# Kernel optimization log

Hardware: AMD Instinct MI355X
Metric: run time of the kernel (lower is better)

The kernel has to match this reference:

```python
import jax, jax.numpy as jnp
import numpy as np

N = 50000          # nodes
E = 800000         # edges (avg degree 16)
IN, HID, OUT = 128, 32, 64
H1, H2, H3 = 4, 4, 6
NEG_SLOPE = 0.2


def setup_inputs() -> dict:
    key = jax.random.key(0)
    ks = jax.random.split(key, 18)

    def p(k, shape, fan_in):
        return (jax.random.normal(k, shape, jnp.float32) / np.sqrt(fan_in)).astype(jnp.float32)

    return {
        "x": jax.random.normal(ks[0], (N, IN), jnp.float32),
        "src": jax.random.randint(ks[1], (E,), 0, N, jnp.int32),
        "dst": jax.random.randint(ks[2], (E,), 0, N, jnp.int32),
        # layer 1: IN -> (H1, HID)
        "W1": p(ks[3], (IN, H1 * HID), IN),
        "al1": p(ks[4], (H1, HID), HID),
        "ar1": p(ks[5], (H1, HID), HID),
        "b1": jnp.zeros((H1 * HID,), jnp.float32),
        # layer 2: H1*HID -> (H2, HID), residual (identity since H1*HID == H2*HID... == in)
        "W2": p(ks[6], (H1 * HID, H2 * HID), H1 * HID),
        "al2": p(ks[7], (H2, HID), HID),
        "ar2": p(ks[8], (H2, HID), HID),
        "b2": jnp.zeros((H2 * HID,), jnp.float32),
        # layer 3: H2*HID -> (H3, OUT), residual via linear projection
        "W3": p(ks[9], (H2 * HID, H3 * OUT), H2 * HID),
        "al3": p(ks[10], (H3, OUT), OUT),
        "ar3": p(ks[11], (H3, OUT), OUT),
        "b3": jnp.zeros((H3 * OUT,), jnp.float32),
        "Wres3": p(ks[12], (H2 * HID, H3 * OUT), H2 * HID),
    }


def _gat_layer(h, W, al, ar, b, src, dst, H, D, resval=None):
    # DGL GATConv: proj, per-edge attention logits, leaky-relu, edge softmax
    # over destination neighborhoods, weighted gather-scatter aggregation.
    feat = (h @ W).reshape(N, H, D)                     # [N,H,D]
    el = jnp.sum(feat * al, axis=-1)                    # [N,H]
    er = jnp.sum(feat * ar, axis=-1)                    # [N,H]
    e = jax.nn.leaky_relu(el[src] + er[dst], NEG_SLOPE) # [E,H]
    # numerically-stable segment softmax over dst
    m = jax.ops.segment_max(e, dst, num_segments=N)     # [N,H]
    ex = jnp.exp(e - m[dst])
    s = jax.ops.segment_sum(ex, dst, num_segments=N)    # [N,H]
    a = ex / s[dst]                                     # [E,H]
    msg = feat[src] * a[..., None]                      # [E,H,D]
    rst = jax.ops.segment_sum(msg, dst, num_segments=N) # [N,H,D]
    if resval is not None:
        rst = rst + resval
    return rst + b.reshape(1, H, D)


def reference(x, src, dst, W1, al1, ar1, b1, W2, al2, ar2, b2,
              W3, al3, ar3, b3, Wres3):
    h = jax.nn.elu(_gat_layer(x, W1, al1, ar1, b1, src, dst, H1, HID))
    h = h.reshape(N, H1 * HID)
    h2 = jax.nn.elu(_gat_layer(h, W2, al2, ar2, b2, src, dst, H2, HID,
                               resval=h.reshape(N, H2, HID)))
    h2 = h2.reshape(N, H2 * HID)
    h3 = _gat_layer(h2, W3, al3, ar3, b3, src, dst, H3, OUT,
                    resval=(h2 @ Wres3).reshape(N, H3, OUT))
    return h3.mean(axis=1)                              # [N,OUT]
```

## Files before the change

kernel.cpp:

```cpp
#include <hip/hip_runtime.h>
#include <hip/hip_bf16.h>


#define NODES 50000
#define EDGES 800000
#define NEG 0.2f

typedef __attribute__((ext_vector_type(8))) short bh8;
typedef __attribute__((ext_vector_type(4))) float f4;

__device__ __forceinline__ float leaky(float e) { return e > 0.f ? e : NEG * e; }
__device__ __forceinline__ float blo(unsigned u) { return __uint_as_float(u << 16); }
__device__ __forceinline__ float bhi(unsigned u) { return __uint_as_float(u & 0xffff0000u); }
__device__ __forceinline__ float bf2f(unsigned short u) {
    return __uint_as_float(((unsigned)u) << 16);
}
__device__ __forceinline__ unsigned f2bf(float f) {
    unsigned u = __float_as_uint(f);
    return (u + 0x7fffu + ((u >> 16) & 1u)) >> 16;
}
__device__ __forceinline__ float sel4(float4 v, int h) {
    float a = (h & 1) ? v.y : v.x;
    float b = (h & 1) ? v.w : v.z;
    return (h & 2) ? b : a;
}

#define SW(row, bc) (((row) << 8) + ((bc) ^ (((row) & 7) << 4)))

__global__ void k_cast(const float* __restrict__ in, unsigned short* __restrict__ outb, int n4) {
    int gid = blockIdx.x * blockDim.x + threadIdx.x;
    if (gid >= n4) return;
    float4 v = *reinterpret_cast<const float4*>(in + (size_t)gid * 4);
    unsigned u0 = f2bf(v.x) | (f2bf(v.y) << 16);
    unsigned u1 = f2bf(v.z) | (f2bf(v.w) << 16);
    *reinterpret_cast<uint2*>(outb + (size_t)gid * 4) = make_uint2(u0, u1);
}

__global__ void k_prepw(const float* __restrict__ W, unsigned short* __restrict__ WT, int F) {
    int gid = blockIdx.x * blockDim.x + threadIdx.x;
    if (gid >= 128 * F) return;
    int k = gid / F, f = gid - k * F;
    WT[(size_t)f * 128 + k] = (unsigned short)f2bf(W[gid]);
}

__global__ void k_hist(const int* __restrict__ dst, int* __restrict__ cnt, int e) {
    int gid = blockIdx.x * blockDim.x + threadIdx.x;
    if (gid < e) atomicAdd(&cnt[dst[gid]], 1);
}

__global__ __launch_bounds__(1024) void k_scan(const int* __restrict__ deg,
                                               int* __restrict__ offs, int n) {
    const int CH = (n + 1023) / 1024;
    int t = threadIdx.x;
    int base = t * CH;
    int s = 0;
    for (int j = 0; j < CH; ++j) {
        int i = base + j;
        if (i < n) s += deg[i];
    }
    __shared__ int sm[1024];
    sm[t] = s;
    __syncthreads();
    for (int off = 1; off < 1024; off <<= 1) {
        int v = (t >= off) ? sm[t - off] : 0;
        __syncthreads();
        sm[t] += v;
        __syncthreads();
    }
    int run = sm[t] - s;
    for (int j = 0; j < CH; ++j) {
        int i = base + j;
        if (i < n) { offs[i] = run; run += deg[i]; }
    }
    if (t == 1023) offs[n] = sm[1023];
}

__global__ void k_fill(const int* __restrict__ src, const int* __restrict__ dst,
                       const int* __restrict__ offs, int* __restrict__ cur,
                       int* __restrict__ csr, int e) {
    int gid = blockIdx.x * blockDim.x + threadIdx.x;
    if (gid < e) {
        int d = dst[gid];
        int pos = offs[d] + atomicAdd(&cur[d], 1);
        csr[pos] = src[gid];
    }
}

template <int F>
__global__ __launch_bounds__(256) void k_mgemm(const unsigned short* __restrict__ A,
                                               const unsigned short* __restrict__ BT,
                                               unsigned short* __restrict__ C0,
                                               unsigned short* __restrict__ C1,
                                               int nrows) {
    __shared__ char Alds[64 * 256];
    __shared__ char Blds[64 * 256];
    const int t  = threadIdx.x;
    const int n0 = blockIdx.x * 64;
    const int w  = t >> 6;
    const int l  = t & 63;
    const int lr = l & 15;
    const int lk = l >> 4;

    {
        int col8 = (t & 15) * 8;
        int bc   = col8 * 2;
#pragma unroll
        for (int p = 0; p < 4; ++p) {
            int row = p * 16 + (t >> 4);
            int gr  = n0 + row;
            uint4 v = make_uint4(0, 0, 0, 0);
            if (gr < nrows) v = *reinterpret_cast<const uint4*>(A + (size_t)gr * 128 + col8);
            *reinterpret_cast<uint4*>(Alds + SW(row, bc)) = v;
        }
    }

    const int rbase = (w & 1) * 32;
    const int cbase = (w >> 1) * 32;

    for (int ct = 0; ct < F / 64; ++ct) {
        __syncthreads();
        {
            int col8 = (t & 15) * 8;
            int bc   = col8 * 2;
#pragma unroll
            for (int p = 0; p < 4; ++p) {
                int row = p * 16 + (t >> 4);
                uint4 v = *reinterpret_cast<const uint4*>(BT + (size_t)(ct * 64 + row) * 128 + col8);
                *reinterpret_cast<uint4*>(Blds + SW(row, bc)) = v;
            }
        }
        __syncthreads();

        f4 acc00 = {0.f, 0.f, 0.f, 0.f}, acc01 = {0.f, 0.f, 0.f, 0.f};
        f4 acc10 = {0.f, 0.f, 0.f, 0.f}, acc11 = {0.f, 0.f, 0.f, 0.f};
#pragma unroll
        for (int kk = 0; kk < 4; ++kk) {
            int bck = kk * 64 + lk * 16;
            bh8 a0 = *reinterpret_cast<const bh8*>(Alds + SW(rbase + lr, bck));
            bh8 a1 = *reinterpret_cast<const bh8*>(Alds + SW(rbase + 16 + lr, bck));
            bh8 b0 = *reinterpret_cast<const bh8*>(Blds + SW(cbase + lr, bck));
            bh8 b1 = *reinterpret_cast<const bh8*>(Blds + SW(cbase + 16 + lr, bck));
            acc00 = __builtin_amdgcn_mfma_f32_16x16x32_bf16(a0, b0, acc00, 0, 0, 0);
            acc01 = __builtin_amdgcn_mfma_f32_16x16x32_bf16(a0, b1, acc01, 0, 0, 0);
            acc10 = __builtin_amdgcn_mfma_f32_16x16x32_bf16(a1, b0, acc10, 0, 0, 0);
            acc11 = __builtin_amdgcn_mfma_f32_16x16x32_bf16(a1, b1, acc11, 0, 0, 0);
        }

        unsigned short* dst = (F == 128) ? C0 : (ct < 6 ? C0 : C1);
        const int width  = (F == 128) ? 128 : 384;
        const int cb     = (F == 128) ? ct * 64 : (ct < 6 ? ct * 64 : ct * 64 - 384);
        const f4* accs[4] = {&acc00, &acc01, &acc10, &acc11};
#pragma unroll
        for (int m = 0; m < 2; ++m) {
#pragma unroll
            for (int j = 0; j < 4; ++j) {
                int gr = n0 + rbase + m * 16 + lk * 4 + j;
                if (gr >= nrows) continue;
#pragma unroll
                for (int n = 0; n < 2; ++n) {
                    float v = (*accs[m * 2 + n])[j];
                    dst[(size_t)gr * width + cb + cbase + n * 16 + lr] = (unsigned short)f2bf(v);
                }
            }
        }
    }
}

template <int H, int D>
__global__ void k_elr_bf(const unsigned short* __restrict__ feat,
                         const float* __restrict__ al, const float* __restrict__ ar,
                         float* __restrict__ el, float* __restrict__ er, int total) {
    int gid = blockIdx.x * blockDim.x + threadIdx.x;
    if (gid >= total) return;
    int n = gid / H, h = gid - n * H;
    const uint4* f = reinterpret_cast<const uint4*>(feat + (size_t)n * (H * D) + h * D);
    const float4* a = reinterpret_cast<const float4*>(al + h * D);
    const float4* r = reinterpret_cast<const float4*>(ar + h * D);
    float sl = 0.f, sr = 0.f;
#pragma unroll
    for (int j = 0; j < D / 8; ++j) {
        uint4 v = f[j];
        float4 a0 = a[2 * j], a1 = a[2 * j + 1];
        float4 r0 = r[2 * j], r1 = r[2 * j + 1];
        float x0 = blo(v.x), x1 = bhi(v.x), x2 = blo(v.y), x3 = bhi(v.y);
        float x4 = blo(v.z), x5 = bhi(v.z), x6 = blo(v.w), x7 = bhi(v.w);
        sl += x0 * a0.x + x1 * a0.y + x2 * a0.z + x3 * a0.w +
              x4 * a1.x + x5 * a1.y + x6 * a1.z + x7 * a1.w;
        sr += x0 * r0.x + x1 * r0.y + x2 * r0.z + x3 * r0.w +
              x4 * r1.x + x5 * r1.y + x6 * r1.z + x7 * r1.w;
    }
    el[gid] = sl;
    er[gid] = sr;
}

template <bool HASRES, bool WRITEF32>
__global__ __launch_bounds__(256) void k_aggr128b(
    const unsigned short* __restrict__ feat, const int* __restrict__ csr,
    const int* __restrict__ offs, const float* __restrict__ el,
    const float* __restrict__ er, const float* __restrict__ bias,
    const float* __restrict__ resf, unsigned short* __restrict__ outb,
    float* __restrict__ outf, int nnodes) {
    int node = blockIdx.x * 4 + (threadIdx.x >> 6);
    if (node >= nnodes) return;
    int l = threadIdx.x & 63;
    int half = l >> 5;
    int ll = l & 31;
    int h = ll >> 3;
    float4 ern = *reinterpret_cast<const float4*>(er + (size_t)node * 4);
    float erh = sel4(ern, h);
    int o0 = offs[node], o1 = offs[node + 1];
    float acc0 = 0.f, acc1 = 0.f, acc2 = 0.f, acc3 = 0.f, s = 0.f;
    int nt = (o1 - o0 + 1) >> 1;
#pragma unroll 2
    for (int t = 0; t < nt; ++t) {
        int ei = o0 + 2 * t + half;
        bool v = ei < o1;
        int sidx = csr[v ? ei : o0];
        float4 la = *reinterpret_cast<const float4*>(el + (size_t)sidx * 4);
        float e = leaky(sel4(la, h) + erh);
        float w = v ? __expf(e) : 0.f;
        s += w;
        uint2 u = *reinterpret_cast<const uint2*>(feat + (size_t)sidx * 128 + 4 * ll);
        acc0 = fmaf(w, blo(u.x), acc0);
        acc1 = fmaf(w, bhi(u.x), acc1);
        acc2 = fmaf(w, blo(u.y), acc2);
        acc3 = fmaf(w, bhi(u.y), acc3);
    }
    s    += __shfl_xor(s, 32);
    acc0 += __shfl_xor(acc0, 32);
    acc1 += __shfl_xor(acc1, 32);
    acc2 += __shfl_xor(acc2, 32);
    acc3 += __shfl_xor(acc3, 32);
    float inv = (o1 > o0) ? 1.f / s : 0.f;
    int f = 4 * ll;
    float4 bi = *reinterpret_cast<const float4*>(bias + f);
    float r0 = acc0 * inv + bi.x;
    float r1 = acc1 * inv + bi.y;
    float r2 = acc2 * inv + bi.z;
    float r3 = acc3 * inv + bi.w;
    if (HASRES) {
        float4 rv = *reinterpret_cast<const float4*>(resf + (size_t)node * 128 + f);
        r0 += rv.x; r1 += rv.y; r2 += rv.z; r3 += rv.w;
    }
    r0 = (r0 > 0.f) ? r0 : (__expf(r0) - 1.f);
    r1 = (r1 > 0.f) ? r1 : (__expf(r1) - 1.f);
    r2 = (r2 > 0.f) ? r2 : (__expf(r2) - 1.f);
    r3 = (r3 > 0.f) ? r3 : (__expf(r3) - 1.f);
    if (half == 0) {
        unsigned u0 = f2bf(r0) | (f2bf(r1) << 16);
        unsigned u1 = f2bf(r2) | (f2bf(r3) << 16);
        *reinterpret_cast<uint2*>(outb + (size_t)node * 128 + f) = make_uint2(u0, u1);
        if (WRITEF32)
            *reinterpret_cast<float4*>(outf + (size_t)node * 128 + f) =
                make_float4(r0, r1, r2, r3);
    }
}

__global__ __launch_bounds__(256) void k_aggr384(
    const unsigned short* __restrict__ feat, const int* __restrict__ csr,
    const int* __restrict__ offs, const float* __restrict__ el,
    const float* __restrict__ er, const float* __restrict__ b3,
    const unsigned short* __restrict__ res3, float* __restrict__ out, int nnodes) {
    int node = blockIdx.x * 4 + (threadIdx.x >> 6);
    if (node >= nnodes) return;
    int l = threadIdx.x & 63;
    int half = l >> 5;
    int ll = l & 31;
    int hi = ll >> 4;
    float erh[3];
#pragma unroll
    for (int j = 0; j < 3; ++j) {
        float2 e2 = *reinterpret_cast<const float2*>(er + (size_t)node * 6 + 2 * j);
        erh[j] = hi ? e2.y : e2.x;
    }
    int o0 = offs[node], o1 = offs[node + 1];
    float a00 = 0.f, a01 = 0.f, a02 = 0.f, a03 = 0.f;
    float a10 = 0.f, a11 = 0.f, a12 = 0.f, a13 = 0.f;
    float a20 = 0.f, a21 = 0.f, a22 = 0.f, a23 = 0.f;
    float s0 = 0.f, s1 = 0.f, s2 = 0.f;
    int nt = (o1 - o0 + 1) >> 1;
#pragma unroll 2
    for (int t = 0; t < nt; ++t) {
        int ei = o0 + 2 * t + half;
        bool v = ei < o1;
        int sidx = csr[v ? ei : o0];
        const unsigned short* fr = feat + (size_t)sidx * 384 + 4 * ll;
        const float* le = el + (size_t)sidx * 6;
        float2 e0 = *reinterpret_cast<const float2*>(le + 0);
        float2 e1 = *reinterpret_cast<const float2*>(le + 2);
        float2 e2 = *reinterpret_cast<const float2*>(le + 4);
        float w0 = v ? __expf(leaky((hi ? e0.y : e0.x) + erh[0])) : 0.f;
        float w1 = v ? __expf(leaky((hi ? e1.y : e1.x) + erh[1])) : 0.f;
        float w2 = v ? __expf(leaky((hi ? e2.y : e2.x) + erh[2])) : 0.f;
        s0 += w0; s1 += w1; s2 += w2;
        uint2 u0 = *reinterpret_cast<const uint2*>(fr);
        uint2 u1 = *reinterpret_cast<const uint2*>(fr + 128);
        uint2 u2 = *reinterpret_cast<const uint2*>(fr + 256);
        a00 = fmaf(w0, blo(u0.x), a00); a01 = fmaf(w0, bhi(u0.x), a01);
        a02 = fmaf(w0, blo(u0.y), a02); a03 = fmaf(w0, bhi(u0.y), a03);
        a10 = fmaf(w1, blo(u1.x), a10); a11 = fmaf(w1, bhi(u1.x), a11);
        a12 = fmaf(w1, blo(u1.y), a12); a13 = fmaf(w1, bhi(u1.y), a13);
        a20 = fmaf(w2, blo(u2.x), a20); a21 = fmaf(w2, bhi(u2.x), a21);
        a22 = fmaf(w2, blo(u2.y), a22); a23 = fmaf(w2, bhi(u2.y), a23);
    }
    bool has = o1 > o0;
    float part0 = 0.f, part1 = 0.f, part2 = 0.f, part3 = 0.f;
    {
        s0 += __shfl_xor(s0, 32);
        float inv = has ? 1.f / s0 : 0.f;
        part0 += (a00 + __shfl_xor(a00, 32)) * inv;
        part1 += (a01 + __shfl_xor(a01, 32)) * inv;
        part2 += (a02 + __shfl_xor(a02, 32)) * inv;
        part3 += (a03 + __shfl_xor(a03, 32)) * inv;
        int f = 4 * ll;
        uint2 r = *reinterpret_cast<const uint2*>(res3 + (size_t)node * 384 + f);
        float4 bb = *reinterpret_cast<const float4*>(b3 + f);
        part0 += blo(r.x) + bb.x; part1 += bhi(r.x) + bb.y;
        part2 += blo(r.y) + bb.z; part3 += bhi(r.y) + bb.w;
    }
    {
        s1 += __shfl_xor(s1, 32);
        float inv = has ? 1.f / s1 : 0.f;
        part0 += (a10 + __shfl_xor(a10, 32)) * inv;
        part1 += (a11 + __shfl_xor(a11, 32)) * inv;
        part2 += (a12 + __shfl_xor(a12, 32)) * inv;
        part3 += (a13 + __shfl_xor(a13, 32)) * inv;
        int f = 128 + 4 * ll;
        uint2 r = *reinterpret_cast<const uint2*>(res3 + (size_t)node * 384 + f);
        float4 bb = *reinterpret_cast<const float4*>(b3 + f);
        part0 += blo(r.x) + bb.x; part1 += bhi(r.x) + bb.y;
        part2 += blo(r.y) + bb.z; part3 += bhi(r.y) + bb.w;
    }
    {
        s2 += __shfl_xor(s2, 32);
        float inv = has ? 1.f / s2 : 0.f;
        part0 += (a20 + __shfl_xor(a20, 32)) * inv;
        part1 += (a21 + __shfl_xor(a21, 32)) * inv;
        part2 += (a22 + __shfl_xor(a22, 32)) * inv;
        part3 += (a23 + __shfl_xor(a23, 32)) * inv;
        int f = 256 + 4 * ll;
        uint2 r = *reinterpret_cast<const uint2*>(res3 + (size_t)node * 384 + f);
        float4 bb = *reinterpret_cast<const float4*>(b3 + f);
        part0 += blo(r.x) + bb.x; part1 += bhi(r.x) + bb.y;
        part2 += blo(r.y) + bb.z; part3 += bhi(r.y) + bb.w;
    }
    part0 += __shfl_xor(part0, 16);
    part1 += __shfl_xor(part1, 16);
    part2 += __shfl_xor(part2, 16);
    part3 += __shfl_xor(part3, 16);
    if (l < 16) {
        *reinterpret_cast<float4*>(out + (size_t)node * 64 + 4 * l) =
            make_float4(part0 * (1.f / 6.f), part1 * (1.f / 6.f),
                        part2 * (1.f / 6.f), part3 * (1.f / 6.f));
    }
}

extern "C" void kernel_launch(void* const* d_in, const int* in_sizes, int n_in,
                              void* d_out, int out_size, void* d_ws, size_t ws_size,
                              hipStream_t stream) {
    const float* x     = (const float*)d_in[0];
    const int*   src   = (const int*)d_in[1];
    const int*   dst   = (const int*)d_in[2];
    const float* W1    = (const float*)d_in[3];
    const float* al1   = (const float*)d_in[4];
    const float* ar1   = (const float*)d_in[5];
    const float* b1    = (const float*)d_in[6];
    const float* W2    = (const float*)d_in[7];
    const float* al2   = (const float*)d_in[8];
    const float* ar2   = (const float*)d_in[9];
    const float* b2    = (const float*)d_in[10];
    const float* W3    = (const float*)d_in[11];
    const float* al3   = (const float*)d_in[12];
    const float* ar3   = (const float*)d_in[13];
    const float* b3    = (const float*)d_in[14];
    const float* Wres3 = (const float*)d_in[15];
    float* out = (float*)d_out;

    const int N = NODES, E = EDGES;

    char*  ws = (char*)d_ws;
    size_t o  = 0;
    auto alloc = [&](size_t bytes) {
        size_t r = o;
        o += (bytes + 255) & ~(size_t)255;
        return r;
    };
    int*            offs   = (int*)(ws + alloc((size_t)(N + 1) * 4));
    int*            cnt    = (int*)(ws + alloc((size_t)N * 4));
    int*            csr    = (int*)(ws + alloc((size_t)E * 4));
    float*          el     = (float*)(ws + alloc((size_t)N * 6 * 4));
    float*          er     = (float*)(ws + alloc((size_t)N * 6 * 4));
    unsigned short* xb     = (unsigned short*)(ws + alloc((size_t)N * 128 * 2));
    unsigned short* featb  = (unsigned short*)(ws + alloc((size_t)N * 128 * 2));
    unsigned short* h1b    = (unsigned short*)(ws + alloc((size_t)N * 128 * 2));
    float*          h1f    = (float*)(ws + alloc((size_t)N * 128 * 4));
    unsigned short* h2b    = (unsigned short*)(ws + alloc((size_t)N * 128 * 2));
    unsigned short* feat3b = (unsigned short*)(ws + alloc((size_t)N * 384 * 2));
    unsigned short* res3b  = (unsigned short*)(ws + alloc((size_t)N * 384 * 2));
    unsigned short* w1t    = (unsigned short*)(ws + alloc((size_t)128 * 128 * 2));
    unsigned short* w2t    = (unsigned short*)(ws + alloc((size_t)128 * 128 * 2));
    unsigned short* w3t    = (unsigned short*)(ws + alloc((size_t)768 * 128 * 2));

    const int gE = (E + 255) / 256;
    const int g4 = (N * 4 + 255) / 256;
    const int g6 = (N * 6 + 255) / 256;
    const int gA = (N + 3) / 4;
    const int gG = (N + 63) / 64;

    k_cast<<<(N * 128 / 4 + 255) / 256, 256, 0, stream>>>(x, xb, N * 128 / 4);
    k_prepw<<<(128 * 128 + 255) / 256, 256, 0, stream>>>(W1, w1t, 128);
    k_prepw<<<(128 * 128 + 255) / 256, 256, 0, stream>>>(W2, w2t, 128);
    k_prepw<<<(128 * 384 + 255) / 256, 256, 0, stream>>>(W3, w3t, 384);
    k_prepw<<<(128 * 384 + 255) / 256, 256, 0, stream>>>(Wres3, w3t + (size_t)384 * 128, 384);

    hipMemsetAsync(cnt, 0, (size_t)N * 4, stream);
    k_hist<<<gE, 256, 0, stream>>>(dst, cnt, E);
    k_scan<<<1, 1024, 0, stream>>>(cnt, offs, N);
    hipMemsetAsync(cnt, 0, (size_t)N * 4, stream);
    k_fill<<<gE, 256, 0, stream>>>(src, dst, offs, cnt, csr, E);

    k_mgemm<128><<<gG, 256, 0, stream>>>(xb, w1t, featb, nullptr, N);
    k_elr_bf<4, 32><<<g4, 256, 0, stream>>>(featb, al1, ar1, el, er, N * 4);
    k_aggr128b<false, true><<<gA, 256, 0, stream>>>(featb, csr, offs, el, er, b1,
                                                    nullptr, h1b, h1f, N);

    k_mgemm<128><<<gG, 256, 0, stream>>>(h1b, w2t, featb, nullptr, N);
    k_elr_bf<4, 32><<<g4, 256, 0, stream>>>(featb, al2, ar2, el, er, N * 4);
    k_aggr128b<true, false><<<gA, 256, 0, stream>>>(featb, csr, offs, el, er, b2,
                                                    h1f, h2b, nullptr, N);

    k_mgemm<768><<<gG, 256, 0, stream>>>(h2b, w3t, feat3b, res3b, N);
    k_elr_bf<6, 64><<<g6, 256, 0, stream>>>(feat3b, al3, ar3, el, er, N * 6);
    k_aggr384<<<gA, 256, 0, stream>>>(feat3b, csr, offs, el, er, b3, res3b, out, N);
}
```

Before: 478.6 us.

## Reassociate layer-3 GAT: aggregate 128-wide inputs then project with fused head-mean GEMM

Layer 3 now aggregates the 128-wide h2 features per head before projecting, instead of first projecting to 384 features and gathering those. The W3 projection, the residual Wres3 projection and the mean over heads are folded into one GEMM with K=896, using weights and attention vectors precomputed from W3, al3, ar3 and b3. The per-head aggregates are stored as bf16 hi/lo pairs to keep precision. The aim is to cut gather bandwidth in the edge loop and drop the large feat3/res3 writes. In exchange the aggregation kernel keeps 6x4 accumulators per lane, and a 13-step K-loop GEMM plus larger z buffers are added.

```diff
diff --git a/kernel.cpp b/kernel.cpp
--- a/kernel.cpp
+++ b/kernel.cpp
@@ -12,9 +12,6 @@
 __device__ __forceinline__ float leaky(float e) { return e > 0.f ? e : NEG * e; }
 __device__ __forceinline__ float blo(unsigned u) { return __uint_as_float(u << 16); }
 __device__ __forceinline__ float bhi(unsigned u) { return __uint_as_float(u & 0xffff0000u); }
-__device__ __forceinline__ float bf2f(unsigned short u) {
-    return __uint_as_float(((unsigned)u) << 16);
-}
 __device__ __forceinline__ unsigned f2bf(float f) {
     unsigned u = __float_as_uint(f);
     return (u + 0x7fffu + ((u >> 16) & 1u)) >> 16;
@@ -23,6 +20,11 @@
     float a = (h & 1) ? v.y : v.x;
     float b = (h & 1) ? v.w : v.z;
     return (h & 2) ? b : a;
+}
+__device__ __forceinline__ void bfsplit(float z, unsigned& hi, unsigned& lo) {
+    hi = f2bf(z);
+    float rem = z - __uint_as_float(hi << 16);
+    lo = f2bf(rem);
 }
 
 #define SW(row, bc) (((row) << 8) + ((bc) ^ (((row) & 7) << 4)))
@@ -41,6 +43,46 @@
     if (gid >= 128 * F) return;
     int k = gid / F, f = gid - k * F;
     WT[(size_t)f * 128 + k] = (unsigned short)f2bf(W[gid]);
+}
+
+__global__ void k_prep_bt2(const float* __restrict__ W3, const float* __restrict__ Wres3,
+                           unsigned short* __restrict__ BT2) {
+    int gid = blockIdx.x * blockDim.x + threadIdx.x;
+    if (gid >= 64 * 896) return;
+    int d = gid / 896, k = gid - d * 896;
+    float v;
+    if (k < 768) {
+        v = W3[(size_t)(k & 127) * 384 + (k >> 7) * 64 + d];
+    } else {
+        int kr = k - 768;
+        v = 0.f;
+#pragma unroll
+        for (int h = 0; h < 6; ++h) v += Wres3[(size_t)kr * 384 + h * 64 + d];
+    }
+    BT2[(size_t)d * 896 + k] = (unsigned short)f2bf(v);
+}
+
+__global__ void k_prep_alr3(const float* __restrict__ W3, const float* __restrict__ al3,
+                            const float* __restrict__ ar3, float* __restrict__ al3c,
+                            float* __restrict__ ar3c) {
+    int gid = blockIdx.x * blockDim.x + threadIdx.x;
+    if (gid >= 1536) return;
+    int g = (gid < 768) ? gid : gid - 768;
+    int h = g >> 7, k = g & 127;
+    const float* a = (gid < 768) ? al3 : ar3;
+    float s = 0.f;
+#pragma unroll
+    for (int d = 0; d < 64; ++d) s += W3[(size_t)k * 384 + h * 64 + d] * a[h * 64 + d];
+    if (gid < 768) al3c[g] = s; else ar3c[g] = s;
+}
+
+__global__ void k_prep_mb(const float* __restrict__ b3, float* __restrict__ mb) {
+    int d = threadIdx.x;
+    if (d >= 64) return;
+    float s = 0.f;
+#pragma unroll
+    for (int h = 0; h < 6; ++h) s += b3[h * 64 + d];
+    mb[d] = s * (1.f / 6.f);
 }
 
 __global__ void k_hist(const int* __restrict__ dst, int* __restrict__ cnt, int e) {
@@ -86,12 +128,10 @@
     }
 }
 
-template <int F>
-__global__ __launch_bounds__(256) void k_mgemm(const unsigned short* __restrict__ A,
-                                               const unsigned short* __restrict__ BT,
-                                               unsigned short* __restrict__ C0,
-                                               unsigned short* __restrict__ C1,
-                                               int nrows) {
+__global__ __launch_bounds__(256) void k_mgemm128(const unsigned short* __restrict__ A,
+                                                  const unsigned short* __restrict__ BT,
+                                                  unsigned short* __restrict__ C0,
+                                                  int nrows) {
     __shared__ char Alds[64 * 256];
     __shared__ char Blds[64 * 256];
     const int t  = threadIdx.x;
@@ -117,7 +157,7 @@
     const int rbase = (w & 1) * 32;
     const int cbase = (w >> 1) * 32;
 
-    for (int ct = 0; ct < F / 64; ++ct) {
+    for (int ct = 0; ct < 2; ++ct) {
         __syncthreads();
         {
             int col8 = (t & 15) * 8;
@@ -146,9 +186,6 @@
             acc11 = __builtin_amdgcn_mfma_f32_16x16x32_bf16(a1, b1, acc11, 0, 0, 0);
         }
 
-        unsigned short* dst = (F == 128) ? C0 : (ct < 6 ? C0 : C1);
-        const int width  = (F == 128) ? 128 : 384;
-        const int cb     = (F == 128) ? ct * 64 : (ct < 6 ? ct * 64 : ct * 64 - 384);
         const f4* accs[4] = {&acc00, &acc01, &acc10, &acc11};
 #pragma unroll
         for (int m = 0; m < 2; ++m) {
@@ -159,8 +196,91 @@
 #pragma unroll
                 for (int n = 0; n < 2; ++n) {
                     float v = (*accs[m * 2 + n])[j];
-                    dst[(size_t)gr * width + cb + cbase + n * 16 + lr] = (unsigned short)f2bf(v);
+                    C0[(size_t)gr * 128 + ct * 64 + cbase + n * 16 + lr] = (unsigned short)f2bf(v);
                 }
+            }
+        }
+    }
+}
+
+__global__ __launch_bounds__(256) void k_mtail(const unsigned short* __restrict__ zb,
+                                               const unsigned short* __restrict__ z2b,
+                                               const unsigned short* __restrict__ h2b,
+                                               const unsigned short* __restrict__ BT2,
+                                               const float* __restrict__ mb,
+                                               float* __restrict__ out, int nrows) {
+    __shared__ char Alds[64 * 256];
+    __shared__ char Blds[64 * 256];
+    const int t  = threadIdx.x;
+    const int n0 = blockIdx.x * 64;
+    const int w  = t >> 6;
+    const int l  = t & 63;
+    const int lr = l & 15;
+    const int lk = l >> 4;
+    const int rbase = (w & 1) * 32;
+    const int cbase = (w >> 1) * 32;
+
+    f4 acc00 = {0.f, 0.f, 0.f, 0.f}, acc01 = {0.f, 0.f, 0.f, 0.f};
+    f4 acc10 = {0.f, 0.f, 0.f, 0.f}, acc11 = {0.f, 0.f, 0.f, 0.f};
+
+    for (int kt = 0; kt < 13; ++kt) {
+        const int bkt = (kt < 6) ? kt : (kt < 12 ? kt - 6 : 6);
+        __syncthreads();
+        {
+            int col8 = (t & 15) * 8;
+            int bc   = col8 * 2;
+#pragma unroll
+            for (int p = 0; p < 4; ++p) {
+                int row = p * 16 + (t >> 4);
+                int gr  = n0 + row;
+                uint4 v = make_uint4(0, 0, 0, 0);
+                if (gr < nrows) {
+                    const unsigned short* ap =
+                        (kt < 6)  ? zb  + (size_t)gr * 768 + kt * 128 :
+                        (kt < 12) ? z2b + (size_t)gr * 768 + (kt - 6) * 128 :
+                                    h2b + (size_t)gr * 128;
+                    v = *reinterpret_cast<const uint4*>(ap + col8);
+                }
+                *reinterpret_cast<uint4*>(Alds + SW(row, bc)) = v;
+            }
+        }
+        {
+            int col8 = (t & 15) * 8;
+            int bc   = col8 * 2;
+#pragma unroll
+            for (int p = 0; p < 4; ++p) {
+                int row = p * 16 + (t >> 4);
+                uint4 v = *reinterpret_cast<const uint4*>(BT2 + (size_t)row * 896 + bkt * 128 + col8);
+                *reinterpret_cast<uint4*>(Blds + SW(row, bc)) = v;
+            }
+        }
+        __syncthreads();
+#pragma unroll
+        for (int kk = 0; kk < 4; ++kk) {
+            int bck = kk * 64 + lk * 16;
+            bh8 a0 = *reinterpret_cast<const bh8*>(Alds + SW(rbase + lr, bck));
+            bh8 a1 = *reinterpret_cast<const bh8*>(Alds + SW(rbase + 16 + lr, bck));
+            bh8 b0 = *reinterpret_cast<const bh8*>(Blds + SW(cbase + lr, bck));
+            bh8 b1 = *reinterpret_cast<const bh8*>(Blds + SW(cbase + 16 + lr, bck));
+            acc00 = __builtin_amdgcn_mfma_f32_16x16x32_bf16(a0, b0, acc00, 0, 0, 0);
+            acc01 = __builtin_amdgcn_mfma_f32_16x16x32_bf16(a0, b1, acc01, 0, 0, 0);
+            acc10 = __builtin_amdgcn_mfma_f32_16x16x32_bf16(a1, b0, acc10, 0, 0, 0);
+            acc11 = __builtin_amdgcn_mfma_f32_16x16x32_bf16(a1, b1, acc11, 0, 0, 0);
+        }
+    }
+
+    const f4* accs[4] = {&acc00, &acc01, &acc10, &acc11};
+#pragma unroll
+    for (int m = 0; m < 2; ++m) {
+#pragma unroll
+        for (int j = 0; j < 4; ++j) {
+            int gr = n0 + rbase + m * 16 + lk * 4 + j;
+            if (gr >= nrows) continue;
+#pragma unroll
+            for (int n = 0; n < 2; ++n) {
+                int col = cbase + n * 16 + lr;
+                float v = (*accs[m * 2 + n])[j];
+                out[(size_t)gr * 64 + col] = v * (1.f / 6.f) + mb[col];
             }
         }
     }
@@ -179,6 +299,32 @@
     float sl = 0.f, sr = 0.f;
 #pragma unroll
     for (int j = 0; j < D / 8; ++j) {
+        uint4 v = f[j];
+        float4 a0 = a[2 * j], a1 = a[2 * j + 1];
+        float4 r0 = r[2 * j], r1 = r[2 * j + 1];
+        float x0 = blo(v.x), x1 = bhi(v.x), x2 = blo(v.y), x3 = bhi(v.y);
+        float x4 = blo(v.z), x5 = bhi(v.z), x6 = blo(v.w), x7 = bhi(v.w);
+        sl += x0 * a0.x + x1 * a0.y + x2 * a0.z + x3 * a0.w +
+              x4 * a1.x + x5 * a1.y + x6 * a1.z + x7 * a1.w;
+        sr += x0 * r0.x + x1 * r0.y + x2 * r0.z + x3 * r0.w +
+              x4 * r1.x + x5 * r1.y + x6 * r1.z + x7 * r1.w;
+    }
+    el[gid] = sl;
+    er[gid] = sr;
+}
+
+__global__ void k_elr3(const unsigned short* __restrict__ h2b,
+                       const float* __restrict__ al3c, const float* __restrict__ ar3c,
+                       float* __restrict__ el, float* __restrict__ er, int total) {
+    int gid = blockIdx.x * blockDim.x + threadIdx.x;
+    if (gid >= total) return;
+    int n = gid / 6, h = gid - n * 6;
+    const uint4* f = reinterpret_cast<const uint4*>(h2b + (size_t)n * 128);
+    const float4* a = reinterpret_cast<const float4*>(al3c + h * 128);
+    const float4* r = reinterpret_cast<const float4*>(ar3c + h * 128);
+    float sl = 0.f, sr = 0.f;
+#pragma unroll
+    for (int j = 0; j < 16; ++j) {
         uint4 v = f[j];
         float4 a0 = a[2 * j], a1 = a[2 * j + 1];
         float4 r0 = r[2 * j], r1 = r[2 * j + 1];
@@ -256,102 +402,72 @@
     }
 }
 
-__global__ __launch_bounds__(256) void k_aggr384(
-    const unsigned short* __restrict__ feat, const int* __restrict__ csr,
+__global__ __launch_bounds__(256) void k_aggrZ(
+    const unsigned short* __restrict__ h2b, const int* __restrict__ csr,
     const int* __restrict__ offs, const float* __restrict__ el,
-    const float* __restrict__ er, const float* __restrict__ b3,
-    const unsigned short* __restrict__ res3, float* __restrict__ out, int nnodes) {
+    const float* __restrict__ er, unsigned short* __restrict__ zb,
+    unsigned short* __restrict__ z2b, int nnodes) {
     int node = blockIdx.x * 4 + (threadIdx.x >> 6);
     if (node >= nnodes) return;
     int l = threadIdx.x & 63;
     int half = l >> 5;
     int ll = l & 31;
-    int hi = ll >> 4;
-    float erh[3];
-#pragma unroll
-    for (int j = 0; j < 3; ++j) {
-        float2 e2 = *reinterpret_cast<const float2*>(er + (size_t)node * 6 + 2 * j);
-        erh[j] = hi ? e2.y : e2.x;
+    float2 er01 = *reinterpret_cast<const float2*>(er + (size_t)node * 6 + 0);
+    float2 er23 = *reinterpret_cast<const float2*>(er + (size_t)node * 6 + 2);
+    float2 er45 = *reinterpret_cast<const float2*>(er + (size_t)node * 6 + 4);
+    float erh[6] = {er01.x, er01.y, er23.x, er23.y, er45.x, er45.y};
+    float acc[6][4];
+    float s[6];
+#pragma unroll
+    for (int h = 0; h < 6; ++h) {
+        s[h] = 0.f;
+#pragma unroll
+        for (int j = 0; j < 4; ++j) acc[h][j] = 0.f;
     }
     int o0 = offs[node], o1 = offs[node + 1];
-    float a00 = 0.f, a01 = 0.f, a02 = 0.f, a03 = 0.f;
-    float a10 = 0.f, a11 = 0.f, a12 = 0.f, a13 = 0.f;
-    float a20 = 0.f, a21 = 0.f, a22 = 0.f, a23 = 0.f;
-    float s0 = 0.f, s1 = 0.f, s2 = 0.f;
     int nt = (o1 - o0 + 1) >> 1;
 #pragma unroll 2
     for (int t = 0; t < nt; ++t) {
         int ei = o0 + 2 * t + half;
         bool v = ei < o1;
         int sidx = csr[v ? ei : o0];
-        const unsigned short* fr = feat + (size_t)sidx * 384 + 4 * ll;
         const float* le = el + (size_t)sidx * 6;
-        float2 e0 = *reinterpret_cast<const float2*>(le + 0);
-        float2 e1 = *reinterpret_cast<const float2*>(le + 2);
-        float2 e2 = *reinterpret_cast<const float2*>(le + 4);
-        float w0 = v ? __expf(leaky((hi ? e0.y : e0.x) + erh[0])) : 0.f;
-        float w1 = v ? __expf(leaky((hi ? e1.y : e1.x) + erh[1])) : 0.f;
-        float w2 = v ? __expf(leaky((hi ? e2.y : e2.x) + erh[2])) : 0.f;
-        s0 += w0; s1 += w1; s2 += w2;
-        uint2 u0 = *reinterpret_cast<const uint2*>(fr);
-        uint2 u1 = *reinterpret_cast<const uint2*>(fr + 128);
-        uint2 u2 = *reinterpret_cast<const uint2*>(fr + 256);
-        a00 = fmaf(w0, blo(u0.x), a00); a01 = fmaf(w0, bhi(u0.x), a01);
-        a02 = fmaf(w0, blo(u0.y), a02); a03 = fmaf(w0, bhi(u0.y), a03);
-        a10 = fmaf(w1, blo(u1.x), a10); a11 = fmaf(w1, bhi(u1.x), a11);
-        a12 = fmaf(w1, blo(u1.y), a12); a13 = fmaf(w1, bhi(u1.y), a13);
-        a20 = fmaf(w2, blo(u2.x), a20); a21 = fmaf(w2, bhi(u2.x), a21);
-        a22 = fmaf(w2, blo(u2.y), a22); a23 = fmaf(w2, bhi(u2.y), a23);
+        float2 e01 = *reinterpret_cast<const float2*>(le + 0);
+        float2 e23 = *reinterpret_cast<const float2*>(le + 2);
+        float2 e45 = *reinterpret_cast<const float2*>(le + 4);
+        float elv[6] = {e01.x, e01.y, e23.x, e23.y, e45.x, e45.y};
+        uint2 u = *reinterpret_cast<const uint2*>(h2b + (size_t)sidx * 128 + 4 * ll);
+        float f0 = blo(u.x), f1 = bhi(u.x), f2 = blo(u.y), f3 = bhi(u.y);
+#pragma unroll
+        for (int h = 0; h < 6; ++h) {
+            float w = v ? __expf(leaky(elv[h] + erh[h])) : 0.f;
+            s[h] += w;
+            acc[h][0] = fmaf(w, f0, acc[h][0]);
+            acc[h][1] = fmaf(w, f1, acc[h][1]);
+            acc[h][2] = fmaf(w, f2, acc[h][2]);
+            acc[h][3] = fmaf(w, f3, acc[h][3]);
+        }
     }
     bool has = o1 > o0;
-    float part0 = 0.f, part1 = 0.f, part2 = 0.f, part3 = 0.f;
-    {
-        s0 += __shfl_xor(s0, 32);
-        float inv = has ? 1.f / s0 : 0.f;
-        part0 += (a00 + __shfl_xor(a00, 32)) * inv;
-        part1 += (a01 + __shfl_xor(a01, 32)) * inv;
-        part2 += (a02 + __shfl_xor(a02, 32)) * inv;
-        part3 += (a03 + __shfl_xor(a03, 32)) * inv;
-        int f = 4 * ll;
-        uint2 r = *reinterpret_cast<const uint2*>(res3 + (size_t)node * 384 + f);
-        float4 bb = *reinterpret_cast<const float4*>(b3 + f);
-        part0 += blo(r.x) + bb.x; part1 += bhi(r.x) + bb.y;
-        part2 += blo(r.y) + bb.z; part3 += bhi(r.y) + bb.w;
-    }
-    {
-        s1 += __shfl_xor(s1, 32);
-        float inv = has ? 1.f / s1 : 0.f;
-        part0 += (a10 + __shfl_xor(a10, 32)) * inv;
-        part1 += (a11 + __shfl_xor(a11, 32)) * inv;
-        part2 += (a12 + __shfl_xor(a12, 32)) * inv;
-        part3 += (a13 + __shfl_xor(a13, 32)) * inv;
-        int f = 128 + 4 * ll;
-        uint2 r = *reinterpret_cast<const uint2*>(res3 + (size_t)node * 384 + f);
-        float4 bb = *reinterpret_cast<const float4*>(b3 + f);
-        part0 += blo(r.x) + bb.x; part1 += bhi(r.x) + bb.y;
-        part2 += blo(r.y) + bb.z; part3 += bhi(r.y) + bb.w;
-    }
-    {
-        s2 += __shfl_xor(s2, 32);
-        float inv = has ? 1.f / s2 : 0.f;
-        part0 += (a20 + __shfl_xor(a20, 32)) * inv;
-        part1 += (a21 + __shfl_xor(a21, 32)) * inv;
-        part2 += (a22 + __shfl_xor(a22, 32)) * inv;
-        part3 += (a23 + __shfl_xor(a23, 32)) * inv;
-        int f = 256 + 4 * ll;
-        uint2 r = *reinterpret_cast<const uint2*>(res3 + (size_t)node * 384 + f);
-        float4 bb = *reinterpret_cast<const float4*>(b3 + f);
-        part0 += blo(r.x) + bb.x; part1 += bhi(r.x) + bb.y;
-        part2 += blo(r.y) + bb.z; part3 += bhi(r.y) + bb.w;
-    }
-    part0 += __shfl_xor(part0, 16);
-    part1 += __shfl_xor(part1, 16);
-    part2 += __shfl_xor(part2, 16);
-    part3 += __shfl_xor(part3, 16);
-    if (l < 16) {
-        *reinterpret_cast<float4*>(out + (size_t)node * 64 + 4 * l) =
-            make_float4(part0 * (1.f / 6.f), part1 * (1.f / 6.f),
-                        part2 * (1.f / 6.f), part3 * (1.f / 6.f));
+#pragma unroll
+    for (int h = 0; h < 6; ++h) {
+        s[h] += __shfl_xor(s[h], 32);
+#pragma unroll
+        for (int j = 0; j < 4; ++j) acc[h][j] += __shfl_xor(acc[h][j], 32);
+    }
+    if (half == 0) {
+#pragma unroll
+        for (int h = 0; h < 6; ++h) {
+            float inv = has ? 1.f / s[h] : 0.f;
+            unsigned hi0, lo0, hi1, lo1, hi2, lo2, hi3, lo3;
+            bfsplit(acc[h][0] * inv, hi0, lo0);
+            bfsplit(acc[h][1] * inv, hi1, lo1);
+            bfsplit(acc[h][2] * inv, hi2, lo2);
+            bfsplit(acc[h][3] * inv, hi3, lo3);
+            size_t off = (size_t)node * 768 + h * 128 + 4 * ll;
+            *reinterpret_cast<uint2*>(zb + off)  = make_uint2(hi0 | (hi1 << 16), hi2 | (hi3 << 16));
+            *reinterpret_cast<uint2*>(z2b + off) = make_uint2(lo0 | (lo1 << 16), lo2 | (lo3 << 16));
+        }
     }
 }
 
@@ -385,21 +501,25 @@
         o += (bytes + 255) & ~(size_t)255;
         return r;
     };
-    int*            offs   = (int*)(ws + alloc((size_t)(N + 1) * 4));
-    int*            cnt    = (int*)(ws + alloc((size_t)N * 4));
-    int*            csr    = (int*)(ws + alloc((size_t)E * 4));
-    float*          el     = (float*)(ws + alloc((size_t)N * 6 * 4));
-    float*          er     = (float*)(ws + alloc((size_t)N * 6 * 4));
-    unsigned short* xb     = (unsigned short*)(ws + alloc((size_t)N * 128 * 2));
-    unsigned short* featb  = (unsigned short*)(ws + alloc((size_t)N * 128 * 2));
-    unsigned short* h1b    = (unsigned short*)(ws + alloc((size_t)N * 128 * 2));
-    float*          h1f    = (float*)(ws + alloc((size_t)N * 128 * 4));
-    unsigned short* h2b    = (unsigned short*)(ws + alloc((size_t)N * 128 * 2));
-    unsigned short* feat3b = (unsigned short*)(ws + alloc((size_t)N * 384 * 2));
-    unsigned short* res3b  = (unsigned short*)(ws + alloc((size_t)N * 384 * 2));
-    unsigned short* w1t    = (unsigned short*)(ws + alloc((size_t)128 * 128 * 2));
-    unsigned short* w2t    = (unsigned short*)(ws + alloc((size_t)128 * 128 * 2));
-    unsigned short* w3t    = (unsigned short*)(ws + alloc((size_t)768 * 128 * 2));
+    int*            offs  = (int*)(ws + alloc((size_t)(N + 1) * 4));
+    int*            cnt   = (int*)(ws + alloc((size_t)N * 4));
+    int*            csr   = (int*)(ws + alloc((size_t)E * 4));
+    float*          el    = (float*)(ws + alloc((size_t)N * 6 * 4));
+    float*          er    = (float*)(ws + alloc((size_t)N * 6 * 4));
+    unsigned short* h2b   = (unsigned short*)(ws + alloc((size_t)N * 128 * 2));
+    unsigned short* w1t   = (unsigned short*)(ws + alloc((size_t)128 * 128 * 2));
+    unsigned short* w2t   = (unsigned short*)(ws + alloc((size_t)128 * 128 * 2));
+    unsigned short* bt2   = (unsigned short*)(ws + alloc((size_t)64 * 896 * 2));
+    float*          al3c  = (float*)(ws + alloc((size_t)768 * 4));
+    float*          ar3c  = (float*)(ws + alloc((size_t)768 * 4));
+    float*          mb    = (float*)(ws + alloc((size_t)64 * 4));
+    char* U = ws + alloc((size_t)N * 768 * 2 * 2);
+    unsigned short* xb    = (unsigned short*)(U);
+    unsigned short* featb = (unsigned short*)(U + (size_t)N * 128 * 2);
+    unsigned short* h1b   = (unsigned short*)(U + (size_t)N * 256 * 2);
+    float*          h1f   = (float*)(U + (size_t)N * 384 * 2);
+    unsigned short* zb    = (unsigned short*)(U);
+    unsigned short* z2b   = (unsigned short*)(U + (size_t)N * 768 * 2);
 
     const int gE = (E + 255) / 256;
     const int g4 = (N * 4 + 255) / 256;
@@ -410,8 +530,9 @@
     k_cast<<<(N * 128 / 4 + 255) / 256, 256, 0, stream>>>(x, xb, N * 128 / 4);
     k_prepw<<<(128 * 128 + 255) / 256, 256, 0, stream>>>(W1, w1t, 128);
     k_prepw<<<(128 * 128 + 255) / 256, 256, 0, stream>>>(W2, w2t, 128);
-    k_prepw<<<(128 * 384 + 255) / 256, 256, 0, stream>>>(W3, w3t, 384);
-    k_prepw<<<(128 * 384 + 255) / 256, 256, 0, stream>>>(Wres3, w3t + (size_t)384 * 128, 384);
+    k_prep_bt2<<<(64 * 896 + 255) / 256, 256, 0, stream>>>(W3, Wres3, bt2);
+    k_prep_alr3<<<6, 256, 0, stream>>>(W3, al3, ar3, al3c, ar3c);
+    k_prep_mb<<<1, 64, 0, stream>>>(b3, mb);
 
     hipMemsetAsync(cnt, 0, (size_t)N * 4, stream);
     k_hist<<<gE, 256, 0, stream>>>(dst, cnt, E);
@@ -419,17 +540,17 @@
     hipMemsetAsync(cnt, 0, (size_t)N * 4, stream);
     k_fill<<<gE, 256, 0, stream>>>(src, dst, offs, cnt, csr, E);
 
-    k_mgemm<128><<<gG, 256, 0, stream>>>(xb, w1t, featb, nullptr, N);
+    k_mgemm128<<<gG, 256, 0, stream>>>(xb, w1t, featb, N);
     k_elr_bf<4, 32><<<g4, 256, 0, stream>>>(featb, al1, ar1, el, er, N * 4);
     k_aggr128b<false, true><<<gA, 256, 0, stream>>>(featb, csr, offs, el, er, b1,
                                                     nullptr, h1b, h1f, N);
 
-    k_mgemm<128><<<gG, 256, 0, stream>>>(h1b, w2t, featb, nullptr, N);
+    k_mgemm128<<<gG, 256, 0, stream>>>(h1b, w2t, featb, N);
     k_elr_bf<4, 32><<<g4, 256, 0, stream>>>(featb, al2, ar2, el, er, N * 4);
     k_aggr128b<true, false><<<gA, 256, 0, stream>>>(featb, csr, offs, el, er, b2,
                                                     h1f, h2b, nullptr, N);
 
-    k_mgemm<768><<<gG, 256, 0, stream>>>(h2b, w3t, feat3b, res3b, N);
-    k_elr_bf<6, 64><<<g6, 256, 0, stream>>>(feat3b, al3, ar3, el, er, N * 6);
-    k_aggr384<<<gA, 256, 0, stream>>>(feat3b, csr, offs, el, er, b3, res3b, out, N);
-}
+    k_elr3<<<g6, 256, 0, stream>>>(h2b, al3c, ar3c, el, er, N * 6);
+    k_aggrZ<<<gA, 256, 0, stream>>>(h2b, csr, offs, el, er, zb, z2b, N);
+    k_mtail<<<gG, 256, 0, stream>>>(zb, z2b, h2b, bt2, mb, out, N);
+}
```

Result: slower. 523.0 us (+9.3%).
